# Kernel tuning notes

Measured on AMD Instinct MI355X. Metric: run time of the kernel, lower is better.

Reference implementation:

```python
import jax, jax.numpy as jnp
import numpy as np

N = 100000
E = 1600000
IN = 128
HEADS = 8
HID = 16  # out_channels // heads
NEG_SLOPE = 0.2


def setup_inputs() -> dict:
    key = jax.random.key(0)
    k1, k2, k3, k4, k5 = jax.random.split(key, 5)
    x = jax.random.normal(k1, (N, IN), dtype=jnp.float32)
    edge_index = jax.random.randint(k2, (2, E), 0, N, dtype=jnp.int32)
    pos = jax.random.uniform(k3, (N,), dtype=jnp.float32)  # positive per-node weights
    W = jax.random.normal(k4, (HEADS * HID, IN), dtype=jnp.float32) * 0.1  # lin.weight
    att = jax.random.normal(k5, (1, HEADS, 2 * HID), dtype=jnp.float32) * 0.1
    return {"x": x, "edge_index": edge_index, "pos": pos, "W": W, "att": att}


def reference(x, edge_index, pos, W, att):
    n = x.shape[0]
    hid = att.shape[-1] // 2
    heads = att.shape[1]
    # linear projection: [N, heads, hid]
    h = (x @ W.T).reshape(n, heads, hid)
    row, col = edge_index[0], edge_index[1]
    # cat([h[row], h[col]], -1) * att -> sum(-1) == h[row].att_l + h[col].att_r
    att_l = att[0, :, :hid]   # [heads, hid]
    att_r = att[0, :, hid:]   # [heads, hid]
    al = jnp.einsum('nhd,hd->nh', h, att_l)  # [N, heads]
    ar = jnp.einsum('nhd,hd->nh', h, att_r)
    alpha = al[row] + ar[col]                # [E, heads]
    alpha = jnp.where(alpha >= 0, alpha, NEG_SLOPE * alpha)  # LeakyReLU
    # softmax_weights: exp, scale by pos[col], normalize by scatter row-sum
    alpha = jnp.exp(alpha) * pos[col][:, None]
    rowsum = jax.ops.segment_sum(alpha, row, num_segments=n)  # [N, heads]
    inv = 1.0 / rowsum + 1e-16
    alpha = alpha * inv[row]
    # weighted scatter-add aggregation
    out = jax.ops.segment_sum(alpha[:, :, None] * h[col], row, num_segments=n)
    return out.reshape(n, heads * hid)  # concat=True
```

## Files before the change

kernel.cpp:

```cpp
#include <hip/hip_runtime.h>
#include <hip/hip_fp16.h>


#define BK    256
#define BSH   8
#define NBMAX 512
#define BCAP  4736
#define EPB   8

typedef _Float16 half8 __attribute__((ext_vector_type(8)));
typedef float    f32x4 __attribute__((ext_vector_type(4)));

__global__ __launch_bounds__(256) void prep_w(
        const float* __restrict__ W, const float* __restrict__ att,
        _Float16* __restrict__ WBh, _Float16* __restrict__ WBl) {
    int i = blockIdx.x * 256 + threadIdx.x;
    if (i >= 4 * 9 * 64 * 8) return;
    const int j    = i & 7;
    const int lane = (i >> 3) & 63;
    const int ctks = i >> 9;
    const int ct   = ctks % 9;
    const int ks   = ctks / 9;
    const int nn   = lane & 15;
    const int kg   = lane >> 4;
    const int k    = ks * 32 + kg * 8 + j;
    float w;
    if (ct < 8) {
        w = W[(ct * 16 + nn) * 128 + k];
    } else {
        const int head = nn & 7;
        const int sel  = nn >> 3;
        float s = 0.f;
        for (int d = 0; d < 16; ++d)
            s += att[head * 32 + sel * 16 + d] * W[(head * 16 + d) * 128 + k];
        w = s;
    }
    const _Float16 hi = (_Float16)w;
    WBh[i] = hi;
    WBl[i] = (_Float16)(w - (float)hi);
}

__global__ __launch_bounds__(256) void node_h(
        const float* __restrict__ x, const _Float16* __restrict__ WBh,
        const _Float16* __restrict__ WBl,
        _Float16* __restrict__ h, float* __restrict__ al,
        _Float16* __restrict__ arh, int n) {
    const int t    = threadIdx.x;
    const int wv   = t >> 6;
    const int lane = t & 63;
    const int m    = lane & 15;
    const int kg   = lane >> 4;
    const int nodeA = blockIdx.x * 64 + wv * 16 + m;
    const bool avalid = nodeA < n;

    f32x4 acc[9];
#pragma unroll
    for (int ct = 0; ct < 9; ++ct) acc[ct] = (f32x4)0.f;

    const half8* bh = (const half8*)WBh;
    const half8* bl = (const half8*)WBl;

#pragma unroll
    for (int ks = 0; ks < 4; ++ks) {
        float xv[8];
        if (avalid) {
            const float4* xp =
                (const float4*)&x[(size_t)nodeA * 128 + ks * 32 + kg * 8];
            *(float4*)&xv[0] = xp[0];
            *(float4*)&xv[4] = xp[1];
        } else {
#pragma unroll
            for (int j = 0; j < 8; ++j) xv[j] = 0.f;
        }
        half8 axh, axl;
#pragma unroll
        for (int j = 0; j < 8; ++j) {
            const _Float16 hi = (_Float16)xv[j];
            axh[j] = hi;
            axl[j] = (_Float16)(xv[j] - (float)hi);
        }
#pragma unroll
        for (int ct = 0; ct < 9; ++ct) {
            const half8 bhv = bh[(ks * 9 + ct) * 64 + lane];
            const half8 blv = bl[(ks * 9 + ct) * 64 + lane];
            acc[ct] = __builtin_amdgcn_mfma_f32_16x16x32_f16(axl, bhv, acc[ct], 0, 0, 0);
            acc[ct] = __builtin_amdgcn_mfma_f32_16x16x32_f16(axh, blv, acc[ct], 0, 0, 0);
            acc[ct] = __builtin_amdgcn_mfma_f32_16x16x32_f16(axh, bhv, acc[ct], 0, 0, 0);
        }
    }

    const int nodeD0 = blockIdx.x * 64 + wv * 16 + kg * 4;
#pragma unroll
    for (int r = 0; r < 4; ++r) {
        const int node = nodeD0 + r;
        if (node < n) {
#pragma unroll
            for (int ct = 0; ct < 8; ++ct)
                h[(size_t)node * 128 + ct * 16 + m] = (_Float16)acc[ct][r];
            if (m < 8) al[node * 8 + m] = acc[8][r];
            else       arh[node * 8 + (m - 8)] = (_Float16)acc[8][r];
        }
    }
}

__global__ __launch_bounds__(512) void bin_edges(
        const int* __restrict__ ei, int* __restrict__ gcur,
        int* __restrict__ bins, int E, int nb) {
    __shared__ int  cnt[NBMAX];
    __shared__ int  basep[NBMAX];
    __shared__ int  lstart[NBMAX];
    __shared__ int2 sorted[512 * EPB];
    const int t    = threadIdx.x;
    const int base = blockIdx.x * (512 * EPB);
    cnt[t] = 0;
    __syncthreads();

    int rr[EPB], off[EPB];
#pragma unroll
    for (int j = 0; j < EPB; ++j) {
        const int e = base + j * 512 + t;
        if (e < E) {
            rr[j]  = ei[e];
            off[j] = atomicAdd(&cnt[rr[j] >> BSH], 1);
        } else rr[j] = -1;
    }
    __syncthreads();
    const int v = cnt[t];
    lstart[t] = v;
    __syncthreads();
    for (int o = 1; o < 512; o <<= 1) {
        const int tmp = (t >= o) ? lstart[t - o] : 0;
        __syncthreads();
        lstart[t] += tmp;
        __syncthreads();
    }
    const int incl = lstart[t];
    __syncthreads();
    lstart[t] = incl - v;
    basep[t]  = (t < nb && v > 0) ? atomicAdd(&gcur[t], v) : 0;
    __syncthreads();

#pragma unroll
    for (int j = 0; j < EPB; ++j) {
        if (rr[j] >= 0) {
            const int e = base + j * 512 + t;
            const int b = rr[j] >> BSH;
            sorted[lstart[b] + off[j]] = make_int2(ei[E + e], rr[j]);
        }
    }
    __syncthreads();

    const int total = lstart[511] + cnt[511];
    for (int i = t; i < total; i += 512) {
        const int2 p = sorted[i];
        const int  b = p.y >> BSH;
        const int  q = basep[b] + i - lstart[b];
        if (q < BCAP)
            bins[(size_t)b * BCAP + q] = p.x | ((p.y & (BK - 1)) << 17);
    }
}

__global__ __launch_bounds__(256) void bucket_fill(
        const int* __restrict__ bins, const int* __restrict__ gcur,
        int* __restrict__ rowstart, int* __restrict__ rowend,
        int* __restrict__ csr, int n, int nb) {
    __shared__ int ld[BK], sc[BK], cur[BK];
    const int b = blockIdx.x, t = threadIdx.x;
    int pv = 0;
    for (int i = t; i < b; i += 256) pv += min(gcur[i], BCAP);
    sc[t] = pv;
    __syncthreads();
    for (int o = 128; o > 0; o >>= 1) {
        if (t < o) sc[t] += sc[t + o];
        __syncthreads();
    }
    const int bbase = sc[0];
    __syncthreads();
    ld[t] = 0;
    __syncthreads();
    const int cnt = min(gcur[b], BCAP);
    const int* bp = bins + (size_t)b * BCAP;
    for (int i = t; i < cnt; i += 256)
        atomicAdd(&ld[((unsigned)bp[i]) >> 17], 1);
    __syncthreads();
    const int v = ld[t];
    sc[t] = v;
    __syncthreads();
    for (int o = 1; o < 256; o <<= 1) {
        const int tmp = (t >= o) ? sc[t - o] : 0;
        __syncthreads();
        sc[t] += tmp;
        __syncthreads();
    }
    const int node = b * BK + t;
    const int s0   = sc[t] - v + bbase;
    cur[t] = s0;
    if (node < n) rowstart[node] = s0;
    __syncthreads();
    for (int i = t; i < cnt; i += 256) {
        const int vv = bp[i];
        const int q  = atomicAdd(&cur[((unsigned)vv) >> 17], 1);
        csr[q] = vv & 0x1FFFF;
    }
    __syncthreads();
    if (node < n) rowend[node] = cur[t];
}

__global__ __launch_bounds__(256) void row_gather(
        const int* __restrict__ csr, const int* __restrict__ rowstart,
        const int* __restrict__ rowend,
        const float* __restrict__ al, const _Float16* __restrict__ arh,
        const float* __restrict__ pos, const _Float16* __restrict__ h,
        float* __restrict__ out, int n) {
    const int r    = (blockIdx.x * 256 + threadIdx.x) >> 6;
    const int lane = threadIdx.x & 63;
    if (r >= n) return;
    const int s = rowstart[r];
    const int e = rowend[r];
    const int sl = lane & 15;
    if (s >= e) {
        if (lane < 16) {
            float4 z = make_float4(0.f, 0.f, 0.f, 0.f);
            *(float4*)&out[(size_t)r * 128 + sl * 8]     = z;
            *(float4*)&out[(size_t)r * 128 + sl * 8 + 4] = z;
        }
        return;
    }
    const int   head = sl >> 1;
    const float al_l = (sl < 8) ? al[r * 8 + sl] : 0.f;
    float acc[8];
#pragma unroll
    for (int i = 0; i < 8; ++i) acc[i] = 0.f;
    float rs = 0.f;
#pragma unroll 2
    for (int j = s; j < e; j += 4) {
        const int  jj    = j + (lane >> 4);
        const bool valid = jj < e;
        const int  c     = csr[valid ? jj : s];
        float av = 0.f;
        if (sl < 8 && valid) {
            float a = al_l + (float)arh[(size_t)c * 8 + sl];
            a  = (a >= 0.f) ? a : 0.2f * a;
            av = __expf(a) * pos[c];
            rs += av;
        }
        const float alpha = __shfl(av, (lane & 48) + head, 64);
        float4 hv = *(const float4*)&h[(size_t)c * 128 + sl * 8];
        const __half2* hp = (const __half2*)&hv;
        const float2 f0 = __half22float2(hp[0]);
        const float2 f1 = __half22float2(hp[1]);
        const float2 f2 = __half22float2(hp[2]);
        const float2 f3 = __half22float2(hp[3]);
        acc[0] = fmaf(alpha, f0.x, acc[0]);
        acc[1] = fmaf(alpha, f0.y, acc[1]);
        acc[2] = fmaf(alpha, f1.x, acc[2]);
        acc[3] = fmaf(alpha, f1.y, acc[3]);
        acc[4] = fmaf(alpha, f2.x, acc[4]);
        acc[5] = fmaf(alpha, f2.y, acc[5]);
        acc[6] = fmaf(alpha, f3.x, acc[6]);
        acc[7] = fmaf(alpha, f3.y, acc[7]);
    }
    rs += __shfl_xor(rs, 16, 64);
    rs += __shfl_xor(rs, 32, 64);
#pragma unroll
    for (int i = 0; i < 8; ++i) {
        acc[i] += __shfl_xor(acc[i], 16, 64);
        acc[i] += __shfl_xor(acc[i], 32, 64);
    }
    const float rsh = __shfl(rs, (lane & 48) + head, 64);
    const float sc  = (rsh != 0.f) ? (1.f / rsh + 1e-16f) : 0.f;
    if (lane < 16) {
        float4 o0 = make_float4(acc[0] * sc, acc[1] * sc, acc[2] * sc, acc[3] * sc);
        float4 o1 = make_float4(acc[4] * sc, acc[5] * sc, acc[6] * sc, acc[7] * sc);
        *(float4*)&out[(size_t)r * 128 + sl * 8]     = o0;
        *(float4*)&out[(size_t)r * 128 + sl * 8 + 4] = o1;
    }
}

extern "C" void kernel_launch(void* const* d_in, const int* in_sizes, int n_in,
                              void* d_out, int out_size, void* d_ws, size_t ws_size,
                              hipStream_t stream) {
    const float* x   = nullptr;
    const int*   ei  = nullptr;
    const float* pos = nullptr;
    const float* W   = nullptr;
    const float* att = nullptr;
    int E2 = 0;
    for (int i = 0; i < n_in; ++i) {
        int s = in_sizes[i];
        if      (s == out_size)        x   = (const float*)d_in[i];
        else if (s == out_size / 128)  pos = (const float*)d_in[i];
        else if (s == 16384)           W   = (const float*)d_in[i];
        else if (s == 256)             att = (const float*)d_in[i];
        else { ei = (const int*)d_in[i]; E2 = s; }
    }
    float* out = (float*)d_out;
    const int N_ = out_size / 128;
    const int E_ = E2 / 2;
    const int NB = (N_ + BK - 1) / BK;

    _Float16* h   = (_Float16*)d_ws;
    float*    al  = (float*)(h + (size_t)N_ * 128);
    _Float16* arh = (_Float16*)(al + (size_t)N_ * 8);
    _Float16* WBh = arh + (size_t)N_ * 8;
    _Float16* WBl = WBh + 18432;
    int* rowstart = (int*)(WBl + 18432);
    int* rowend   = rowstart + N_;
    int* gcur     = rowend + N_;
    int* csr      = gcur + NBMAX;
    int* bins     = csr + E_;

    hipMemsetAsync(gcur, 0, (size_t)NBMAX * sizeof(int), stream);

    prep_w<<<72, 256, 0, stream>>>(W, att, WBh, WBl);
    node_h<<<(N_ + 63) / 64, 256, 0, stream>>>(x, WBh, WBl, h, al, arh, N_);
    bin_edges<<<(E_ + 512 * EPB - 1) / (512 * EPB), 512, 0, stream>>>(
        ei, gcur, bins, E_, NB);
    bucket_fill<<<NB, 256, 0, stream>>>(bins, gcur, rowstart, rowend,
                                        csr, N_, NB);
    row_gather<<<(N_ * 64 + 255) / 256, 256, 0, stream>>>(
        csr, rowstart, rowend, al, arh, pos, h, out, N_);
}
```

Baseline: 259.9 us.

## Process 8 edges per iteration in row_gather and cache bucket in LDS

row_gather now computes attention weights for 8 edges at once, using all 64 lanes (8 edges x 8 heads) instead of only 8 of every 16 lanes. It then performs two 4-edge feature-accumulation passes per iteration. bucket_fill stages each bucket's entries in shared memory so the second pass reads LDS instead of global memory, and row start/end are packed into a single int2 to save a load. This adds an extra csr load per sub-pass and roughly 19KB of LDS per bucket_fill block, which may reduce occupancy.

Result: faster. 252.1 us (-3.0%).

```diff
diff --git a/kernel.cpp b/kernel.cpp
--- a/kernel.cpp
+++ b/kernel.cpp
@@ -162,8 +162,8 @@
 
 __global__ __launch_bounds__(256) void bucket_fill(
         const int* __restrict__ bins, const int* __restrict__ gcur,
-        int* __restrict__ rowstart, int* __restrict__ rowend,
-        int* __restrict__ csr, int n, int nb) {
+        int2* __restrict__ rowse, int* __restrict__ csr, int n, int nb) {
+    __shared__ int sh[BCAP];
     __shared__ int ld[BK], sc[BK], cur[BK];
     const int b = blockIdx.x, t = threadIdx.x;
     int pv = 0;
@@ -180,8 +180,11 @@
     __syncthreads();
     const int cnt = min(gcur[b], BCAP);
     const int* bp = bins + (size_t)b * BCAP;
-    for (int i = t; i < cnt; i += 256)
-        atomicAdd(&ld[((unsigned)bp[i]) >> 17], 1);
+    for (int i = t; i < cnt; i += 256) {
+        const int v = bp[i];
+        sh[i] = v;
+        atomicAdd(&ld[((unsigned)v) >> 17], 1);
+    }
     __syncthreads();
     const int v = ld[t];
     sc[t] = v;
@@ -195,28 +198,26 @@
     const int node = b * BK + t;
     const int s0   = sc[t] - v + bbase;
     cur[t] = s0;
-    if (node < n) rowstart[node] = s0;
     __syncthreads();
     for (int i = t; i < cnt; i += 256) {
-        const int vv = bp[i];
+        const int vv = sh[i];
         const int q  = atomicAdd(&cur[((unsigned)vv) >> 17], 1);
         csr[q] = vv & 0x1FFFF;
     }
     __syncthreads();
-    if (node < n) rowend[node] = cur[t];
+    if (node < n) rowse[node] = make_int2(s0, cur[t]);
 }
 
 __global__ __launch_bounds__(256) void row_gather(
-        const int* __restrict__ csr, const int* __restrict__ rowstart,
-        const int* __restrict__ rowend,
+        const int* __restrict__ csr, const int2* __restrict__ rowse,
         const float* __restrict__ al, const _Float16* __restrict__ arh,
         const float* __restrict__ pos, const _Float16* __restrict__ h,
         float* __restrict__ out, int n) {
     const int r    = (blockIdx.x * 256 + threadIdx.x) >> 6;
     const int lane = threadIdx.x & 63;
     if (r >= n) return;
-    const int s = rowstart[r];
-    const int e = rowend[r];
+    const int2 se = rowse[r];
+    const int s = se.x, e = se.y;
     const int sl = lane & 15;
     if (s >= e) {
         if (lane < 16) {
@@ -226,40 +227,65 @@
         }
         return;
     }
-    const int   head = sl >> 1;
-    const float al_l = (sl < 8) ? al[r * 8 + sl] : 0.f;
+    const int hd  = lane & 7;
+    const int es  = lane >> 3;
+    const int esA = lane >> 4;
+    const float al_h = al[r * 8 + hd];
     float acc[8];
 #pragma unroll
     for (int i = 0; i < 8; ++i) acc[i] = 0.f;
     float rs = 0.f;
-#pragma unroll 2
-    for (int j = s; j < e; j += 4) {
-        const int  jj    = j + (lane >> 4);
-        const bool valid = jj < e;
-        const int  c     = csr[valid ? jj : s];
+    for (int j = s; j < e; j += 8) {
+        const int  j1 = j + es;
+        const bool v1 = j1 < e;
+        const int  c1 = csr[v1 ? j1 : s];
         float av = 0.f;
-        if (sl < 8 && valid) {
-            float a = al_l + (float)arh[(size_t)c * 8 + sl];
+        if (v1) {
+            float a = al_h + (float)arh[(size_t)c1 * 8 + hd];
             a  = (a >= 0.f) ? a : 0.2f * a;
-            av = __expf(a) * pos[c];
+            av = __expf(a) * pos[c1];
             rs += av;
         }
-        const float alpha = __shfl(av, (lane & 48) + head, 64);
-        float4 hv = *(const float4*)&h[(size_t)c * 128 + sl * 8];
-        const __half2* hp = (const __half2*)&hv;
-        const float2 f0 = __half22float2(hp[0]);
-        const float2 f1 = __half22float2(hp[1]);
-        const float2 f2 = __half22float2(hp[2]);
-        const float2 f3 = __half22float2(hp[3]);
-        acc[0] = fmaf(alpha, f0.x, acc[0]);
-        acc[1] = fmaf(alpha, f0.y, acc[1]);
-        acc[2] = fmaf(alpha, f1.x, acc[2]);
-        acc[3] = fmaf(alpha, f1.y, acc[3]);
-        acc[4] = fmaf(alpha, f2.x, acc[4]);
-        acc[5] = fmaf(alpha, f2.y, acc[5]);
-        acc[6] = fmaf(alpha, f3.x, acc[6]);
-        acc[7] = fmaf(alpha, f3.y, acc[7]);
-    }
+        {
+            const int  jA = j + esA;
+            const int  cA = csr[(jA < e) ? jA : s];
+            const float alpha = __shfl(av, esA * 8 + (sl >> 1), 64);
+            float4 hv = *(const float4*)&h[(size_t)cA * 128 + sl * 8];
+            const __half2* hp = (const __half2*)&hv;
+            const float2 f0 = __half22float2(hp[0]);
+            const float2 f1 = __half22float2(hp[1]);
+            const float2 f2 = __half22float2(hp[2]);
+            const float2 f3 = __half22float2(hp[3]);
+            acc[0] = fmaf(alpha, f0.x, acc[0]);
+            acc[1] = fmaf(alpha, f0.y, acc[1]);
+            acc[2] = fmaf(alpha, f1.x, acc[2]);
+            acc[3] = fmaf(alpha, f1.y, acc[3]);
+            acc[4] = fmaf(alpha, f2.x, acc[4]);
+            acc[5] = fmaf(alpha, f2.y, acc[5]);
+            acc[6] = fmaf(alpha, f3.x, acc[6]);
+            acc[7] = fmaf(alpha, f3.y, acc[7]);
+        }
+        {
+            const int  jB = j + 4 + esA;
+            const int  cB = csr[(jB < e) ? jB : s];
+            const float alpha = __shfl(av, 32 + esA * 8 + (sl >> 1), 64);
+            float4 hv = *(const float4*)&h[(size_t)cB * 128 + sl * 8];
+            const __half2* hp = (const __half2*)&hv;
+            const float2 f0 = __half22float2(hp[0]);
+            const float2 f1 = __half22float2(hp[1]);
+            const float2 f2 = __half22float2(hp[2]);
+            const float2 f3 = __half22float2(hp[3]);
+            acc[0] = fmaf(alpha, f0.x, acc[0]);
+            acc[1] = fmaf(alpha, f0.y, acc[1]);
+            acc[2] = fmaf(alpha, f1.x, acc[2]);
+            acc[3] = fmaf(alpha, f1.y, acc[3]);
+            acc[4] = fmaf(alpha, f2.x, acc[4]);
+            acc[5] = fmaf(alpha, f2.y, acc[5]);
+            acc[6] = fmaf(alpha, f3.x, acc[6]);
+            acc[7] = fmaf(alpha, f3.y, acc[7]);
+        }
+    }
+    rs += __shfl_xor(rs, 8, 64);
     rs += __shfl_xor(rs, 16, 64);
     rs += __shfl_xor(rs, 32, 64);
 #pragma unroll
@@ -267,7 +293,7 @@
         acc[i] += __shfl_xor(acc[i], 16, 64);
         acc[i] += __shfl_xor(acc[i], 32, 64);
     }
-    const float rsh = __shfl(rs, (lane & 48) + head, 64);
+    const float rsh = __shfl(rs, (lane & 15) >> 1, 64);
     const float sc  = (rsh != 0.f) ? (1.f / rsh + 1e-16f) : 0.f;
     if (lane < 16) {
         float4 o0 = make_float4(acc[0] * sc, acc[1] * sc, acc[2] * sc, acc[3] * sc);
@@ -304,9 +330,8 @@
     _Float16* arh = (_Float16*)(al + (size_t)N_ * 8);
     _Float16* WBh = arh + (size_t)N_ * 8;
     _Float16* WBl = WBh + 18432;
-    int* rowstart = (int*)(WBl + 18432);
-    int* rowend   = rowstart + N_;
-    int* gcur     = rowend + N_;
+    int2* rowse   = (int2*)(WBl + 18432);
+    int* gcur     = (int*)(rowse + N_);
     int* csr      = gcur + NBMAX;
     int* bins     = csr + E_;
 
@@ -316,8 +341,7 @@
     node_h<<<(N_ + 63) / 64, 256, 0, stream>>>(x, WBh, WBl, h, al, arh, N_);
     bin_edges<<<(E_ + 512 * EPB - 1) / (512 * EPB), 512, 0, stream>>>(
         ei, gcur, bins, E_, NB);
-    bucket_fill<<<NB, 256, 0, stream>>>(bins, gcur, rowstart, rowend,
-                                        csr, N_, NB);
+    bucket_fill<<<NB, 256, 0, stream>>>(bins, gcur, rowse, csr, N_, NB);
     row_gather<<<(N_ * 64 + 255) / 256, 256, 0, stream>>>(
-        csr, rowstart, rowend, al, arh, pos, h, out, N_);
-}
+        csr, rowse, al, arh, pos, h, out, N_);
+}
```
